# Optimization experiments

Hardware: AMD Instinct MI355X
Metric: run time of the kernel (lower is better)

## Reference

```python
import jax, jax.numpy as jnp
import numpy as np

BATCH, IN_F, OUT_F = 4096, 1024, 1024


def setup_inputs() -> dict:
    key = jax.random.key(0)
    kx, kw = jax.random.split(key)
    x = jax.random.normal(kx, (BATCH, IN_F, 4), dtype=jnp.float32)
    weight = jax.random.normal(kw, (OUT_F, IN_F, 4), dtype=jnp.float32) * 0.01
    bias = jnp.zeros((OUT_F, 4), dtype=jnp.float32)
    return {"x": x, "weight": weight, "bias": bias}


def reference(x, weight, bias):
    # x: (batch, in, 4) quaternions; weight: (out, in, 4); bias: (out, 4)
    # Hamilton product broadcast over (batch, out, in) then summed over in ==
    # 16 signed real GEMMs contracting the `in` dimension.
    ar, ai, aj, ak = x[..., 0], x[..., 1], x[..., 2], x[..., 3]          # (b, i)
    br, bi, bj, bk = weight[..., 0], weight[..., 1], weight[..., 2], weight[..., 3]  # (o, i)

    mm = lambda a, w: jnp.einsum('bi,oi->bo', a, w)

    out_r = mm(ar, br) - mm(ai, bi) - mm(aj, bj) - mm(ak, bk)
    out_i = mm(ar, bi) + mm(ai, br) + mm(aj, bk) - mm(ak, bj)
    out_j = mm(ar, bj) - mm(ai, bk) + mm(aj, br) + mm(ak, bi)
    out_k = mm(ar, bk) + mm(ai, bj) - mm(aj, bi) + mm(ak, br)

    out = jnp.stack([out_r, out_i, out_j, out_k], axis=-1)  # (b, o, 4)
    return out + bias
```

## Files before the change

kernel.cpp:

```cpp
#include <hip/hip_runtime.h>


typedef __bf16 bf16x8 __attribute__((ext_vector_type(8)));
typedef float floatx4 __attribute__((ext_vector_type(4)));

constexpr int M = 4096;
constexpr int N = 4096;
constexpr int K = 4096;
constexpr int BM = 128, BN = 128, BK = 32;

constexpr int CVT_BLOCKS = (M * K / 8) / 256;
constexpr int EXP_BLOCKS = (1024 * 1024 / 2) / 256;

#define WAIT_VM4 0x0F74
#define WAIT_VM0 0x0F70
#define BARRIER() asm volatile("s_barrier" ::: "memory")

__global__ void prep_kernel(const float* __restrict__ x, const float* __restrict__ w,
                            __bf16* __restrict__ A, __bf16* __restrict__ Wb) {
    const int b = blockIdx.x;
    if (b < CVT_BLOCKS) {
        const size_t i = (size_t)b * 256 + threadIdx.x;
        const float4* xp = (const float4*)x;
        float4 a = xp[2 * i];
        float4 c = xp[2 * i + 1];
        bf16x8 v;
        v[0] = (__bf16)a.x; v[1] = (__bf16)a.y; v[2] = (__bf16)a.z; v[3] = (__bf16)a.w;
        v[4] = (__bf16)c.x; v[5] = (__bf16)c.y; v[6] = (__bf16)c.z; v[7] = (__bf16)c.w;
        *(bf16x8*)(A + 8 * i) = v;
    } else {
        const int idx = (b - CVT_BLOCKS) * 256 + threadIdx.x;
        const int o  = idx >> 9;
        const int ip = (idx & 511) * 2;
        float4 q0 = ((const float4*)w)[o * 1024 + ip];
        float4 q1 = ((const float4*)w)[o * 1024 + ip + 1];
        __bf16* base = Wb + (size_t)(o * 4) * K + ip * 4;
        bf16x8 r;
        r[0] = (__bf16)q0.x; r[1] = (__bf16)(-q0.y); r[2] = (__bf16)(-q0.z); r[3] = (__bf16)(-q0.w);
        r[4] = (__bf16)q1.x; r[5] = (__bf16)(-q1.y); r[6] = (__bf16)(-q1.z); r[7] = (__bf16)(-q1.w);
        *(bf16x8*)(base) = r;
        r[0] = (__bf16)q0.y; r[1] = (__bf16)q0.x; r[2] = (__bf16)q0.w; r[3] = (__bf16)(-q0.z);
        r[4] = (__bf16)q1.y; r[5] = (__bf16)q1.x; r[6] = (__bf16)q1.w; r[7] = (__bf16)(-q1.z);
        *(bf16x8*)(base + (size_t)K) = r;
        r[0] = (__bf16)q0.z; r[1] = (__bf16)(-q0.w); r[2] = (__bf16)q0.x; r[3] = (__bf16)q0.y;
        r[4] = (__bf16)q1.z; r[5] = (__bf16)(-q1.w); r[6] = (__bf16)q1.x; r[7] = (__bf16)q1.y;
        *(bf16x8*)(base + (size_t)2 * K) = r;
        r[0] = (__bf16)q0.w; r[1] = (__bf16)q0.z; r[2] = (__bf16)(-q0.y); r[3] = (__bf16)q0.x;
        r[4] = (__bf16)q1.w; r[5] = (__bf16)q1.z; r[6] = (__bf16)(-q1.y); r[7] = (__bf16)q1.x;
        *(bf16x8*)(base + (size_t)3 * K) = r;
    }
}

__device__ __forceinline__ void gload_lds16(const __bf16* g, __bf16* l) {
    __builtin_amdgcn_global_load_lds(
        (const __attribute__((address_space(1))) void*)g,
        (__attribute__((address_space(3))) void*)l, 16, 0, 0);
}

__global__ void qgemm_kernel(const __bf16* __restrict__ A,
                             const __bf16* __restrict__ B,
                             const float* __restrict__ bias,
                             float* __restrict__ C) {
    __shared__ __bf16 As[3][BM][BK];
    __shared__ __bf16 Bs[3][BN][BK];

    const int tid  = threadIdx.x;
    const int wave = tid >> 6;
    const int lane = tid & 63;

    const int bid = blockIdx.x;
    const int xcd = bid & 7;
    const int q   = bid >> 3;
    const int ty  = (xcd >> 2) * 16 + (q & 15);
    const int tx  = (xcd & 3) * 8 + (q >> 4);
    const int bm = ty * BM;
    const int bn = tx * BN;

    const int wm = (wave & 1) * 64;
    const int wn = (wave >> 1) * 64;

    const int ldrow = lane >> 2;
    const int sc    = (lane & 3) ^ ((lane >> 3) & 3);
    const int ldcol = sc * 8;

    const __bf16* ag0 = A + (size_t)(bm + wave * 16 + ldrow) * K + ldcol;
    const __bf16* ag1 = ag0 + (size_t)64 * K;
    const __bf16* bg0 = B + (size_t)(bn + wave * 16 + ldrow) * K + ldcol;
    const __bf16* bg1 = bg0 + (size_t)64 * K;

    floatx4 acc[4][4] = {};

    const int fl  = lane & 15;
    const int fq  = lane >> 4;
    const int fco = (fq ^ ((fl >> 1) & 3)) * 8;

    auto issue = [&](int b, int k) {
        const int off = k * BK;
        gload_lds16(ag0 + off, &As[b][wave * 16][0]);
        gload_lds16(ag1 + off, &As[b][64 + wave * 16][0]);
        gload_lds16(bg0 + off, &Bs[b][wave * 16][0]);
        gload_lds16(bg1 + off, &Bs[b][64 + wave * 16][0]);
    };

    auto step = [&](int k, int br, int bw, bool doi) {
        bf16x8 af[4], bfr[4];
#pragma unroll
        for (int t = 0; t < 4; ++t)
            af[t] = *(const bf16x8*)&As[br][wm + t * 16 + fl][fco];
#pragma unroll
        for (int t = 0; t < 4; ++t)
            bfr[t] = *(const bf16x8*)&Bs[br][wn + t * 16 + fl][fco];
        if (doi) issue(bw, k + 2);
#pragma unroll
        for (int mt = 0; mt < 4; ++mt)
#pragma unroll
            for (int nt = 0; nt < 4; ++nt)
                acc[mt][nt] = __builtin_amdgcn_mfma_f32_16x16x32_bf16(
                    af[mt], bfr[nt], acc[mt][nt], 0, 0, 0);
    };

    issue(0, 0);
    issue(1, 1);

    for (int k = 0; k < 126; k += 3) {
        __builtin_amdgcn_s_waitcnt(WAIT_VM4);
        BARRIER();
        step(k, 0, 2, true);
        __builtin_amdgcn_s_waitcnt(WAIT_VM4);
        BARRIER();
        step(k + 1, 1, 0, true);
        __builtin_amdgcn_s_waitcnt(WAIT_VM4);
        BARRIER();
        step(k + 2, 2, 1, true);
    }
    __builtin_amdgcn_s_waitcnt(WAIT_VM4);
    BARRIER();
    step(126, 0, 0, false);
    __builtin_amdgcn_s_waitcnt(WAIT_VM0);
    BARRIER();
    step(127, 1, 0, false);

#pragma unroll
    for (int mt = 0; mt < 4; ++mt) {
        const int row = bm + wm + mt * 16 + fq * 4;
#pragma unroll
        for (int nt = 0; nt < 4; ++nt) {
            const int col = bn + wn + nt * 16 + fl;
            const float bv = bias[col];
            float* cp = C + (size_t)row * N + col;
#pragma unroll
            for (int r = 0; r < 4; ++r)
                cp[(size_t)r * N] = acc[mt][nt][r] + bv;
        }
    }
}

extern "C" void kernel_launch(void* const* d_in, const int* in_sizes, int n_in,
                              void* d_out, int out_size, void* d_ws, size_t ws_size,
                              hipStream_t stream) {
    const float* x    = (const float*)d_in[0];
    const float* w    = (const float*)d_in[1];
    const float* bias = (const float*)d_in[2];
    float* out = (float*)d_out;

    __bf16* Abf  = (__bf16*)d_ws;
    __bf16* Wbig = (__bf16*)((char*)d_ws + (size_t)M * K * 2);

    prep_kernel<<<CVT_BLOCKS + EXP_BLOCKS, 256, 0, stream>>>(x, w, Abf, Wbig);

    qgemm_kernel<<<1024, 256, 0, stream>>>(Abf, Wbig, bias, out);
}
```

Measured before the change: 286.8 us.

## Enlarge GEMM tiles to 256x256x64 with 8 waves and interleaved prefetch

Switches the bf16 GEMM from 128x128x32 tiles with 4 waves and triple buffering to 256x256x64 tiles with 8 waves, double-buffered LDS, and a phased schedule. The A loads for the next tile and the B loads two tiles ahead are spread across four sub-steps, and MFMA blocks are wrapped in setprio. The aim is more reuse per byte loaded and fewer barriers per FLOP. In exchange it uses much more LDS and registers per block and launches only 256 blocks, which may underfill the 256 CUs and leaves the B-buffer reuse timing fragile.

After: 281.5 us. Within noise of the previous version (-1.8%).

```diff
diff --git a/kernel.cpp b/kernel.cpp
--- a/kernel.cpp
+++ b/kernel.cpp
@@ -7,7 +7,8 @@
 constexpr int M = 4096;
 constexpr int N = 4096;
 constexpr int K = 4096;
-constexpr int BM = 128, BN = 128, BK = 32;
+constexpr int BM = 256, BN = 256, BK = 64;
+constexpr int TILES = K / BK;
 
 constexpr int CVT_BLOCKS = (M * K / 8) / 256;
 constexpr int EXP_BLOCKS = (1024 * 1024 / 2) / 256;
@@ -57,12 +58,12 @@
         (__attribute__((address_space(3))) void*)l, 16, 0, 0);
 }
 
-__global__ void qgemm_kernel(const __bf16* __restrict__ A,
-                             const __bf16* __restrict__ B,
-                             const float* __restrict__ bias,
-                             float* __restrict__ C) {
-    __shared__ __bf16 As[3][BM][BK];
-    __shared__ __bf16 Bs[3][BN][BK];
+__global__ __launch_bounds__(512) void qgemm_kernel(const __bf16* __restrict__ A,
+                                                    const __bf16* __restrict__ B,
+                                                    const float* __restrict__ bias,
+                                                    float* __restrict__ C) {
+    __shared__ __bf16 As[2][BM][BK];
+    __shared__ __bf16 Bs[2][BN][BK];
 
     const int tid  = threadIdx.x;
     const int wave = tid >> 6;
@@ -71,77 +72,88 @@
     const int bid = blockIdx.x;
     const int xcd = bid & 7;
     const int q   = bid >> 3;
-    const int ty  = (xcd >> 2) * 16 + (q & 15);
-    const int tx  = (xcd & 3) * 8 + (q >> 4);
-    const int bm = ty * BM;
-    const int bn = tx * BN;
+    const int tm  = (xcd >> 2) * 8 + (q & 7);
+    const int tn  = (xcd & 3) * 4 + (q >> 3);
+    const int bm  = tm * BM;
+    const int bn  = tn * BN;
 
-    const int wm = (wave & 1) * 64;
-    const int wn = (wave >> 1) * 64;
+    const int wm = (wave >> 2) * 128;
+    const int wn = (wave & 3) * 64;
 
-    const int ldrow = lane >> 2;
-    const int sc    = (lane & 3) ^ ((lane >> 3) & 3);
-    const int ldcol = sc * 8;
+    const int srow = wave * 16 + (lane >> 3);
+    const int schk = ((lane & 7) ^ (lane >> 3)) * 8;
+    const __bf16* agA = A + (size_t)(bm + srow) * K + schk;
+    const __bf16* agB = B + (size_t)(bn + srow) * K + schk;
 
-    const __bf16* ag0 = A + (size_t)(bm + wave * 16 + ldrow) * K + ldcol;
-    const __bf16* ag1 = ag0 + (size_t)64 * K;
-    const __bf16* bg0 = B + (size_t)(bn + wave * 16 + ldrow) * K + ldcol;
-    const __bf16* bg1 = bg0 + (size_t)64 * K;
-
-    floatx4 acc[4][4] = {};
+    auto issueA = [&](int buf, int h, int t) {
+        const __bf16* g = agA + (size_t)h * 128 * K + t * BK;
+        gload_lds16(g,                 &As[buf][h * 128 + wave * 16][0]);
+        gload_lds16(g + (size_t)8 * K, &As[buf][h * 128 + wave * 16 + 8][0]);
+    };
+    auto issueB = [&](int buf, int h, int t) {
+        const __bf16* g = agB + (size_t)h * 128 * K + t * BK;
+        gload_lds16(g,                 &Bs[buf][h * 128 + wave * 16][0]);
+        gload_lds16(g + (size_t)8 * K, &Bs[buf][h * 128 + wave * 16 + 8][0]);
+    };
 
     const int fl  = lane & 15;
     const int fq  = lane >> 4;
-    const int fco = (fq ^ ((fl >> 1) & 3)) * 8;
+    const int fx7 = fl & 7;
+    const int eo0 = (fq ^ fx7) * 8;
+    const int eo1 = ((4 + fq) ^ fx7) * 8;
 
-    auto issue = [&](int b, int k) {
-        const int off = k * BK;
-        gload_lds16(ag0 + off, &As[b][wave * 16][0]);
-        gload_lds16(ag1 + off, &As[b][64 + wave * 16][0]);
-        gload_lds16(bg0 + off, &Bs[b][wave * 16][0]);
-        gload_lds16(bg1 + off, &Bs[b][64 + wave * 16][0]);
-    };
+    floatx4 acc[8][4] = {};
+    bf16x8 bF[4][2];
 
-    auto step = [&](int k, int br, int bw, bool doi) {
-        bf16x8 af[4], bfr[4];
-#pragma unroll
-        for (int t = 0; t < 4; ++t)
-            af[t] = *(const bf16x8*)&As[br][wm + t * 16 + fl][fco];
-#pragma unroll
-        for (int t = 0; t < 4; ++t)
-            bfr[t] = *(const bf16x8*)&Bs[br][wn + t * 16 + fl][fco];
-        if (doi) issue(bw, k + 2);
-#pragma unroll
-        for (int mt = 0; mt < 4; ++mt)
-#pragma unroll
-            for (int nt = 0; nt < 4; ++nt)
-                acc[mt][nt] = __builtin_amdgcn_mfma_f32_16x16x32_bf16(
-                    af[mt], bfr[nt], acc[mt][nt], 0, 0, 0);
-    };
-
-    issue(0, 0);
-    issue(1, 1);
-
-    for (int k = 0; k < 126; k += 3) {
-        __builtin_amdgcn_s_waitcnt(WAIT_VM4);
-        BARRIER();
-        step(k, 0, 2, true);
-        __builtin_amdgcn_s_waitcnt(WAIT_VM4);
-        BARRIER();
-        step(k + 1, 1, 0, true);
-        __builtin_amdgcn_s_waitcnt(WAIT_VM4);
-        BARRIER();
-        step(k + 2, 2, 1, true);
-    }
+    issueA(0, 0, 0); issueA(0, 1, 0);
+    issueB(0, 0, 0); issueB(0, 1, 0);
+    issueB(1, 0, 1); issueB(1, 1, 1);
     __builtin_amdgcn_s_waitcnt(WAIT_VM4);
     BARRIER();
-    step(126, 0, 0, false);
-    __builtin_amdgcn_s_waitcnt(WAIT_VM0);
-    BARRIER();
-    step(127, 1, 0, false);
+
+    for (int t = 0; t < TILES; ++t) {
+        const int b = t & 1;
+#pragma unroll
+        for (int p = 0; p < 4; ++p) {
+            bf16x8 aL0 = *(const bf16x8*)&As[b][wm + (2 * p) * 16 + fl][eo0];
+            bf16x8 aL1 = *(const bf16x8*)&As[b][wm + (2 * p) * 16 + fl][eo1];
+            bf16x8 aH0 = *(const bf16x8*)&As[b][wm + (2 * p + 1) * 16 + fl][eo0];
+            bf16x8 aH1 = *(const bf16x8*)&As[b][wm + (2 * p + 1) * 16 + fl][eo1];
+            if (p == 0) {
+#pragma unroll
+                for (int nt = 0; nt < 4; ++nt) {
+                    bF[nt][0] = *(const bf16x8*)&Bs[b][wn + nt * 16 + fl][eo0];
+                    bF[nt][1] = *(const bf16x8*)&Bs[b][wn + nt * 16 + fl][eo1];
+                }
+            }
+            if (p == 0 && t + 1 < TILES) issueA(b ^ 1, 0, t + 1);
+            if (p == 1 && t + 1 < TILES) issueA(b ^ 1, 1, t + 1);
+            if (p == 2 && t + 2 < TILES) issueB(b, 0, t + 2);
+            if (p == 3 && t + 2 < TILES) issueB(b, 1, t + 2);
+            BARRIER();
+            __builtin_amdgcn_s_setprio(1);
+#pragma unroll
+            for (int nt = 0; nt < 4; ++nt) {
+                acc[2 * p][nt]     = __builtin_amdgcn_mfma_f32_16x16x32_bf16(
+                    aL0, bF[nt][0], acc[2 * p][nt], 0, 0, 0);
+                acc[2 * p + 1][nt] = __builtin_amdgcn_mfma_f32_16x16x32_bf16(
+                    aH0, bF[nt][0], acc[2 * p + 1][nt], 0, 0, 0);
+                acc[2 * p][nt]     = __builtin_amdgcn_mfma_f32_16x16x32_bf16(
+                    aL1, bF[nt][1], acc[2 * p][nt], 0, 0, 0);
+                acc[2 * p + 1][nt] = __builtin_amdgcn_mfma_f32_16x16x32_bf16(
+                    aH1, bF[nt][1], acc[2 * p + 1][nt], 0, 0, 0);
+            }
+            __builtin_amdgcn_s_setprio(0);
+            if (p == 3) {
+                if (t + 2 < TILES) __builtin_amdgcn_s_waitcnt(WAIT_VM4);
+                else               __builtin_amdgcn_s_waitcnt(WAIT_VM0);
+            }
+            BARRIER();
+        }
+    }
 
 #pragma unroll
-    for (int mt = 0; mt < 4; ++mt) {
+    for (int mt = 0; mt < 8; ++mt) {
         const int row = bm + wm + mt * 16 + fq * 4;
 #pragma unroll
         for (int nt = 0; nt < 4; ++nt) {
@@ -168,5 +180,5 @@
 
     prep_kernel<<<CVT_BLOCKS + EXP_BLOCKS, 256, 0, stream>>>(x, w, Abf, Wbig);
 
-    qgemm_kernel<<<1024, 256, 0, stream>>>(Abf, Wbig, bias, out);
+    qgemm_kernel<<<256, 512, 0, stream>>>(Abf, Wbig, bias, out);
 }
```
